# Optimization experiments

Hardware: AMD Instinct MI355X
Metric: run time of the kernel (lower is better)

## Reference

```python
import jax, jax.numpy as jnp
import numpy as np

H0, H1, NL, B, S = 2048, 1024, 8, 2, 2048

def _linear(x, w, b):
    return jnp.einsum('bsd,od->bso', x, w) + b

def setup_inputs() -> dict:
    key = jax.random.key(0)
    ks = jax.random.split(key, 32)
    d = {
        'z':    jax.random.normal(ks[0], (B, S, H0), jnp.float32),
        'act0': jax.random.normal(ks[1], (B, S, H0), jnp.float32),
        'act1': jax.random.normal(ks[2], (B, S, H0), jnp.float32),
        'attmask': jax.random.randint(ks[3], (B, S), 0, 2, jnp.int32),
        'dproj_w': jax.random.normal(ks[4], (H1, H0), jnp.float32) * 0.02,
        'dproj_b': jnp.zeros((H1,), jnp.float32),
        'uproj_w': jax.random.normal(ks[5], (H0, H1), jnp.float32) * 0.02,
        'uproj_b': jnp.zeros((H0,), jnp.float32),
        'wq_w': jax.random.normal(ks[6], (NL, H1, H1), jnp.float32) * 0.02,
        'wq_b': jnp.zeros((NL, H1), jnp.float32),
        'wk_w': jax.random.normal(ks[7], (NL, H1, H1), jnp.float32) * 0.02,
        'wk_b': jnp.zeros((NL, H1), jnp.float32),
        'wv_w': jax.random.normal(ks[8], (NL, H1, H1), jnp.float32) * 0.02,
        'wv_b': jnp.zeros((NL, H1), jnp.float32),
        'mlp1_w': jax.random.normal(ks[9], (NL, 4 * H1, H1), jnp.float32) * 0.02,
        'mlp1_b': jnp.zeros((NL, 4 * H1), jnp.float32),
        'mlp2_w': jax.random.normal(ks[10], (NL, H1, 4 * H1), jnp.float32) * 0.02,
        'mlp2_b': jnp.zeros((NL, H1), jnp.float32),
    }
    return d

def _ladder_fwd(z, act0, act1, attmask, dproj_w, dproj_b, uproj_w, uproj_b,
                wq_w, wq_b, wk_w, wk_b, wv_w, wv_b,
                mlp1_w, mlp1_b, mlp2_w, mlp2_b):
    seq = z.shape[1]
    scale = 1.0 / jnp.sqrt(jnp.float32(H1))
    causal = jnp.tril(jnp.ones((seq, seq), bool))  # [S,S]
    pad = (attmask != 0)[:, None, :]               # [B,1,S] key padding mask
    neg = jnp.float32(-1e9)

    def ladsatt(i, x):
        Q = _linear(x, wq_w[i], wq_b[i])
        K = _linear(x, wk_w[i], wk_b[i])
        V = _linear(x, wv_w[i], wv_b[i])
        scores = jnp.einsum('bqd,bkd->bqk', Q, K) * scale
        scores = jnp.where(causal[None], scores, neg)
        scores = jnp.where(pad, scores, neg)
        w = jax.nn.softmax(scores, axis=-1)
        return jnp.einsum('bqk,bkd->bqd', w, V)

    def mlp(i, x):
        h = jax.nn.relu(_linear(x, mlp1_w[i], mlp1_b[i]))
        return _linear(h, mlp2_w[i], mlp2_b[i])

    rs = _linear(act0, dproj_w, dproj_b)
    rs = rs + ladsatt(0, rs)
    rs = rs + mlp(0, rs)
    rs = rs + _linear(act1, dproj_w, dproj_b)
    rs = rs + ladsatt(1, rs)
    rs = rs + mlp(1, rs)
    for i in range(2, NL):
        rs = rs + ladsatt(i, rs)
        rs = rs + mlp(i, rs)
    return _linear(rs, uproj_w, uproj_b) + z

def reference(z, act0, act1, attmask, dproj_w, dproj_b, uproj_w, uproj_b,
              wq_w, wq_b, wk_w, wk_b, wv_w, wv_b,
              mlp1_w, mlp1_b, mlp2_w, mlp2_b):
    return _ladder_fwd(z, act0, act1, attmask, dproj_w, dproj_b, uproj_w, uproj_b,
                       wq_w, wq_b, wk_w, wk_b, wv_w, wv_b,
                       mlp1_w, mlp1_b, mlp2_w, mlp2_b)
```

## Files before the change

### kernel.cpp

```cpp
#include <hip/hip_runtime.h>
#include <cstdint>


typedef unsigned short u16;
typedef __attribute__((ext_vector_type(8))) __bf16 bf16x8;
typedef __attribute__((ext_vector_type(4))) float f32x4;

#define DI __device__ __forceinline__

constexpr int BB = 2, SSQ = 2048, HH0 = 2048, HH1 = 1024, NLAY = 8, HH4 = 4096;
constexpr int MM = BB * SSQ;

DI float bf2f(u16 h) {
  union { uint32_t u; float f; } x; x.u = ((uint32_t)h) << 16; return x.f;
}
DI u16 f2bf(float f) {
  union { float f; uint32_t u; } x; x.f = f;
  uint32_t u = x.u;
  return (u16)((u + 0x7fffu + ((u >> 16) & 1u)) >> 16);
}

enum {
  FB_BIAS = 1, FB_RES = 2, FB_RELU = 4, FB_F32 = 8, FB_SPLIT = 16,
  FB_CSKIP = 32, FB_CKLOOP = 64
};

template <int F, int KSP>
__global__ __launch_bounds__(256) void gemm_split(
    const u16* __restrict__ Ah, const u16* __restrict__ Al, long sAz, int lda,
    const u16* __restrict__ Bh, const u16* __restrict__ Bl, long sBz, int ldb,
    const float* __restrict__ bias, const float* __restrict__ resF,
    float* Cf, u16* Ch, u16* Cl, long sCz, int ldc, int K, long pstride) {
  int gx = gridDim.x, gy = gridDim.y, gz = gridDim.z;
  long o = blockIdx.x + (long)gx * (blockIdx.y + (long)gy * blockIdx.z);
  long nwg = (long)gx * gy * gz;
  long cq = nwg >> 3, cr = nwg & 7;
  long xcd = o & 7, cidx = o >> 3;
  long sl = (xcd < cr ? xcd * (cq + 1) : cr * (cq + 1) + (xcd - cr) * cq) + cidx;
  int bx = (int)(sl % gx);
  long tt = sl / gx;
  int by = (int)(tt % gy);
  int bzf = (int)(tt / gy);
  int NB = gz / KSP;
  int bz = bzf % NB;
  int ks = bzf / NB;

  if ((F & FB_CSKIP) && bx > by) return;

  __shared__ __align__(16) u16 Sbuf[2][4][128 * 32];

  int tid = threadIdx.x;
  int lane = tid & 63;
  int wave = tid >> 6;
  int wr = (wave >> 1) << 6;
  int wc = (wave & 1) << 6;
  int lrow = lane & 15;
  int kg = lane >> 4;
  int kc8 = (kg ^ ((lrow >> 1) & 3)) << 3;

  const u16* Abh = Ah + (long)bz * sAz + ((long)(by << 7)) * lda;
  const u16* Abl = Al + (long)bz * sAz + ((long)(by << 7)) * lda;
  const u16* Bbh = Bh + (long)bz * sBz + ((long)(bx << 7)) * ldb;
  const u16* Bbl = Bl + (long)bz * sBz + ((long)(bx << 7)) * ldb;

  int nKtot = (F & FB_CKLOOP) ? ((by + 1) << 2) : (K >> 5);
  int kbeg = (KSP > 1) ? (ks * nKtot) / KSP : 0;
  int kend = (KSP > 1) ? ((ks + 1) * nKtot) / KSP : nKtot;

  f32x4 acc[4][4] = {};

  auto STAGE = [&](int buf, int kt) {
    int k0 = kt << 5;
#pragma unroll
    for (int it = 0; it < 2; ++it) {
      int sidx = (it << 8) + tid;
      int r = sidx >> 2;
      int jsw = (sidx & 3) ^ ((r >> 1) & 3);
      long goff = (long)r * lda + (k0 + (jsw << 3));
      long gofB = (long)r * ldb + (k0 + (jsw << 3));
      int loff = sidx << 3;
      __builtin_amdgcn_global_load_lds(
          (__attribute__((address_space(1))) void*)(Abh + goff),
          (__attribute__((address_space(3))) void*)(&Sbuf[buf][0][loff]), 16, 0, 0);
      __builtin_amdgcn_global_load_lds(
          (__attribute__((address_space(1))) void*)(Abl + goff),
          (__attribute__((address_space(3))) void*)(&Sbuf[buf][1][loff]), 16, 0, 0);
      __builtin_amdgcn_global_load_lds(
          (__attribute__((address_space(1))) void*)(Bbh + gofB),
          (__attribute__((address_space(3))) void*)(&Sbuf[buf][2][loff]), 16, 0, 0);
      __builtin_amdgcn_global_load_lds(
          (__attribute__((address_space(1))) void*)(Bbl + gofB),
          (__attribute__((address_space(3))) void*)(&Sbuf[buf][3][loff]), 16, 0, 0);
    }
  };

  auto COMPUTE = [&](int buf) {
    bf16x8 afh[4], bfh[4], bfl[4];
#pragma unroll
    for (int mi = 0; mi < 4; ++mi)
      afh[mi] = *(const bf16x8*)&Sbuf[buf][0][((wr + (mi << 4) + lrow) << 5) + kc8];
#pragma unroll
    for (int ni = 0; ni < 4; ++ni) {
      bfh[ni] = *(const bf16x8*)&Sbuf[buf][2][((wc + (ni << 4) + lrow) << 5) + kc8];
      bfl[ni] = *(const bf16x8*)&Sbuf[buf][3][((wc + (ni << 4) + lrow) << 5) + kc8];
    }
#pragma unroll
    for (int mi = 0; mi < 4; ++mi)
#pragma unroll
      for (int ni = 0; ni < 4; ++ni) {
        acc[mi][ni] = __builtin_amdgcn_mfma_f32_16x16x32_bf16(
            afh[mi], bfh[ni], acc[mi][ni], 0, 0, 0);
        acc[mi][ni] = __builtin_amdgcn_mfma_f32_16x16x32_bf16(
            afh[mi], bfl[ni], acc[mi][ni], 0, 0, 0);
      }
    bf16x8 afl[4];
#pragma unroll
    for (int mi = 0; mi < 4; ++mi)
      afl[mi] = *(const bf16x8*)&Sbuf[buf][1][((wr + (mi << 4) + lrow) << 5) + kc8];
#pragma unroll
    for (int mi = 0; mi < 4; ++mi)
#pragma unroll
      for (int ni = 0; ni < 4; ++ni)
        acc[mi][ni] = __builtin_amdgcn_mfma_f32_16x16x32_bf16(
            afl[mi], bfh[ni], acc[mi][ni], 0, 0, 0);
  };

  STAGE(0, kbeg);
  int cur = 0;
  for (int kt = kbeg; kt < kend; ++kt) {
    bool more = (kt + 1 < kend);
    if (more) STAGE(cur ^ 1, kt + 1);
    if (more) asm volatile("s_waitcnt vmcnt(8)" ::: "memory");
    else      asm volatile("s_waitcnt vmcnt(0)" ::: "memory");
    __builtin_amdgcn_s_barrier();
    asm volatile("" ::: "memory");
    COMPUTE(cur);
    asm volatile("" ::: "memory");
    __builtin_amdgcn_s_barrier();
    asm volatile("" ::: "memory");
    cur ^= 1;
  }

  int m0 = (by << 7) + wr + (kg << 2);
  int n0 = (bx << 7) + wc;
#pragma unroll
  for (int mi = 0; mi < 4; ++mi) {
#pragma unroll
    for (int ni = 0; ni < 4; ++ni) {
      int col = n0 + (ni << 4) + lrow;
      float bv = 0.f;
      if ((KSP == 1) && (F & FB_BIAS)) bv = bias[col];
      int rb = m0 + (mi << 4);
#pragma unroll
      for (int r = 0; r < 4; ++r) {
        float v = acc[mi][ni][r];
        long ci = (long)bz * sCz + (long)(rb + r) * ldc + col;
        if constexpr (KSP > 1) {
          Cf[(long)ks * pstride + ci] = v;
        } else {
          v += bv;
          if (F & FB_RELU) v = fmaxf(v, 0.f);
          if (F & FB_RES) v += resF[ci];
          if (F & FB_F32) Cf[ci] = v;
          if (F & FB_SPLIT) {
            u16 h = f2bf(v);
            Ch[ci] = h;
            Cl[ci] = f2bf(v - bf2f(h));
          }
        }
      }
    }
  }
}

template <int F, int KSP>
__global__ __launch_bounds__(512, 2) void gemm_big(
    const u16* __restrict__ Ah, const u16* __restrict__ Al, int lda,
    const u16* __restrict__ Bh, const u16* __restrict__ Bl, int ldb,
    const float* __restrict__ bias,
    float* Cf, u16* Ch, u16* Cl, int ldc, int K, long pstride) {
  int gx = gridDim.x, gy = gridDim.y, gz = gridDim.z;
  long o = blockIdx.x + (long)gx * (blockIdx.y + (long)gy * blockIdx.z);
  long nwg = (long)gx * gy * gz;
  long cq = nwg >> 3, cr = nwg & 7;
  long xcd = o & 7, cidx = o >> 3;
  long sl = (xcd < cr ? xcd * (cq + 1) : cr * (cq + 1) + (xcd - cr) * cq) + cidx;
  int bx = (int)(sl % gx);
  long tt = sl / gx;
  int by = (int)(tt % gy);
  int ks = (int)(tt / gy);

  __shared__ __align__(16) u16 Sbuf[2][4][256 * 32];

  int tid = threadIdx.x;
  int lane = tid & 63;
  int wave = tid >> 6;
  int wm = (wave >> 2) << 7;
  int wn = (wave & 3) << 6;
  int lrow = lane & 15;
  int kg = lane >> 4;
  int kc8 = (kg ^ ((lrow >> 1) & 3)) << 3;

  const u16* Abh = Ah + ((long)(by << 8)) * lda;
  const u16* Abl = Al + ((long)(by << 8)) * lda;
  const u16* Bbh = Bh + ((long)(bx << 8)) * ldb;
  const u16* Bbl = Bl + ((long)(bx << 8)) * ldb;

  int nKtot = K >> 5;
  int kbeg = (KSP > 1) ? (ks * nKtot) / KSP : 0;
  int kend = (KSP > 1) ? ((ks + 1) * nKtot) / KSP : nKtot;

  f32x4 acc[8][4] = {};

  auto STAGE = [&](int buf, int kt) {
    int k0 = kt << 5;
#pragma unroll
    for (int it = 0; it < 2; ++it) {
      int sidx = (it << 9) + tid;
      int r = sidx >> 2;
      int jsw = (sidx & 3) ^ ((r >> 1) & 3);
      long goff = (long)r * lda + (k0 + (jsw << 3));
      long gofB = (long)r * ldb + (k0 + (jsw << 3));
      int loff = sidx << 3;
      __builtin_amdgcn_global_load_lds(
          (__attribute__((address_space(1))) void*)(Abh + goff),
          (__attribute__((address_space(3))) void*)(&Sbuf[buf][0][loff]), 16, 0, 0);
      __builtin_amdgcn_global_load_lds(
          (__attribute__((address_space(1))) void*)(Abl + goff),
          (__attribute__((address_space(3))) void*)(&Sbuf[buf][1][loff]), 16, 0, 0);
      __builtin_amdgcn_global_load_lds(
          (__attribute__((address_space(1))) void*)(Bbh + gofB),
          (__attribute__((address_space(3))) void*)(&Sbuf[buf][2][loff]), 16, 0, 0);
      __builtin_amdgcn_global_load_lds(
          (__attribute__((address_space(1))) void*)(Bbl + gofB),
          (__attribute__((address_space(3))) void*)(&Sbuf[buf][3][loff]), 16, 0, 0);
    }
  };

  auto COMPUTE = [&](int buf) {
    bf16x8 bfh[4], bfl[4];
#pragma unroll
    for (int ni = 0; ni < 4; ++ni) {
      int brow = wn + (ni << 4) + lrow;
      bfh[ni] = *(const bf16x8*)&Sbuf[buf][2][(brow << 5) + kc8];
      bfl[ni] = *(const bf16x8*)&Sbuf[buf][3][(brow << 5) + kc8];
    }
#pragma unroll
    for (int mi = 0; mi < 8; ++mi) {
      int arow = wm + (mi << 4) + lrow;
      bf16x8 ah = *(const bf16x8*)&Sbuf[buf][0][(arow << 5) + kc8];
      bf16x8 al = *(const bf16x8*)&Sbuf[buf][1][(arow << 5) + kc8];
#pragma unroll
      for (int ni = 0; ni < 4; ++ni) {
        acc[mi][ni] = __builtin_amdgcn_mfma_f32_16x16x32_bf16(
            ah, bfh[ni], acc[mi][ni], 0, 0, 0);
        acc[mi][ni] = __builtin_amdgcn_mfma_f32_16x16x32_bf16(
            ah, bfl[ni], acc[mi][ni], 0, 0, 0);
        acc[mi][ni] = __builtin_amdgcn_mfma_f32_16x16x32_bf16(
            al, bfh[ni], acc[mi][ni], 0, 0, 0);
      }
    }
  };

  STAGE(0, kbeg);
  int cur = 0;
  for (int kt = kbeg; kt < kend; ++kt) {
    bool more = (kt + 1 < kend);
    if (more) STAGE(cur ^ 1, kt + 1);
    if (more) asm volatile("s_waitcnt vmcnt(8)" ::: "memory");
    else      asm volatile("s_waitcnt vmcnt(0)" ::: "memory");
    __builtin_amdgcn_s_barrier();
    asm volatile("" ::: "memory");
    COMPUTE(cur);
    asm volatile("" ::: "memory");
    __builtin_amdgcn_s_barrier();
    asm volatile("" ::: "memory");
    cur ^= 1;
  }

  int m0 = (by << 8) + wm + (kg << 2);
  int n0 = (bx << 8) + wn;
#pragma unroll
  for (int mi = 0; mi < 8; ++mi) {
#pragma unroll
    for (int ni = 0; ni < 4; ++ni) {
      int col = n0 + (ni << 4) + lrow;
      float bv = 0.f;
      if ((KSP == 1) && (F & FB_BIAS)) bv = bias[col];
      int rb = m0 + (mi << 4);
#pragma unroll
      for (int r = 0; r < 4; ++r) {
        float v = acc[mi][ni][r];
        long ci = (long)(rb + r) * ldc + col;
        if constexpr (KSP > 1) {
          Cf[(long)ks * pstride + ci] = v;
        } else {
          v += bv;
          if (F & FB_RELU) v = fmaxf(v, 0.f);
          if (F & FB_F32) Cf[ci] = v;
          if (F & FB_SPLIT) {
            u16 h = f2bf(v);
            Ch[ci] = h;
            Cl[ci] = f2bf(v - bf2f(h));
          }
        }
      }
    }
  }
}

template <int KSP, bool RES>
__global__ void reduce_split(const float* __restrict__ p,
                             const float* __restrict__ bias,
                             float* __restrict__ rs, u16* __restrict__ xh,
                             u16* __restrict__ xl) {
  long i = ((long)blockIdx.x * 256 + threadIdx.x) << 2;
  int col = (int)(i & 1023);
  constexpr long PSTR = (long)MM * HH1;
  float4 v;
  v.x = bias[col]; v.y = bias[col + 1]; v.z = bias[col + 2]; v.w = bias[col + 3];
#pragma unroll
  for (int j = 0; j < KSP; ++j) {
    float4 a = *(const float4*)(p + i + j * PSTR);
    v.x += a.x; v.y += a.y; v.z += a.z; v.w += a.w;
  }
  if (RES) {
    float4 r0 = *(const float4*)(rs + i);
    v.x += r0.x; v.y += r0.y; v.z += r0.z; v.w += r0.w;
  }
  *(float4*)(rs + i) = v;
  ushort4 h, l;
  h.x = f2bf(v.x); l.x = f2bf(v.x - bf2f(h.x));
  h.y = f2bf(v.y); l.y = f2bf(v.y - bf2f(h.y));
  h.z = f2bf(v.z); l.z = f2bf(v.z - bf2f(h.z));
  h.w = f2bf(v.w); l.w = f2bf(v.w - bf2f(h.w));
  *(ushort4*)(xh + i) = h;
  *(ushort4*)(xl + i) = l;
}

__global__ void split_kernel(const float* __restrict__ src, u16* __restrict__ hi,
                             u16* __restrict__ lo) {
  long i = ((long)blockIdx.x * 256 + threadIdx.x) << 2;
  float4 v = *(const float4*)(src + i);
  ushort4 h, l;
  h.x = f2bf(v.x); l.x = f2bf(v.x - bf2f(h.x));
  h.y = f2bf(v.y); l.y = f2bf(v.y - bf2f(h.y));
  h.z = f2bf(v.z); l.z = f2bf(v.z - bf2f(h.z));
  h.w = f2bf(v.w); l.w = f2bf(v.w - bf2f(h.w));
  *(ushort4*)(hi + i) = h;
  *(ushort4*)(lo + i) = l;
}

__global__ void concat_bias(const float* __restrict__ qb, const float* __restrict__ kb,
                            const float* __restrict__ vb, float* __restrict__ dst) {
  int j = blockIdx.x * 256 + threadIdx.x;
  float v = (j < 1024) ? qb[j] : ((j < 2048) ? kb[j - 1024] : vb[j - 2048]);
  dst[j] = v;
}

__global__ void deg_kernel(const int* __restrict__ am, int* __restrict__ deg) {
  int i = blockIdx.x * 256 + threadIdx.x;
  int b = i >> 11, q = i & 2047;
  const int* a = am + b * SSQ;
  int any = 0;
  for (int k = 0; k <= q; ++k) any |= (a[k] != 0);
  deg[i] = !any;
}

__global__ void transpose_v2(const u16* __restrict__ Vh, const u16* __restrict__ Vl,
                             int sld, u16* __restrict__ VTh, u16* __restrict__ VTl) {
  __shared__ u16 th[64][68];
  __shared__ u16 tl[64][68];
  int b = blockIdx.z;
  int c0 = blockIdx.x << 6;
  int r0 = blockIdx.y << 6;
  int tr = threadIdx.x >> 4, tc = threadIdx.x & 15;
  long sbase = ((long)(b * SSQ + r0)) * sld + c0;
#pragma unroll
  for (int j = 0; j < 4; ++j) {
    int r = (j << 4) + tr;
    ushort4 uh = *(const ushort4*)(Vh + sbase + (long)r * sld + (tc << 2));
    ushort4 ul = *(const ushort4*)(Vl + sbase + (long)r * sld + (tc << 2));
    th[r][(tc << 2) + 0] = uh.x; th[r][(tc << 2) + 1] = uh.y;
    th[r][(tc << 2) + 2] = uh.z; th[r][(tc << 2) + 3] = uh.w;
    tl[r][(tc << 2) + 0] = ul.x; tl[r][(tc << 2) + 1] = ul.y;
    tl[r][(tc << 2) + 2] = ul.z; tl[r][(tc << 2) + 3] = ul.w;
  }
  __syncthreads();
  long dbase = ((long)b * HH1 + c0) * SSQ + r0;
#pragma unroll
  for (int j = 0; j < 4; ++j) {
    int c = (j << 4) + tr;
    ushort4 uh, ul;
    uh.x = th[(tc << 2) + 0][c]; uh.y = th[(tc << 2) + 1][c];
    uh.z = th[(tc << 2) + 2][c]; uh.w = th[(tc << 2) + 3][c];
    ul.x = tl[(tc << 2) + 0][c]; ul.y = tl[(tc << 2) + 1][c];
    ul.z = tl[(tc << 2) + 2][c]; ul.w = tl[(tc << 2) + 3][c];
    *(ushort4*)(VTh + dbase + (long)c * SSQ + (tc << 2)) = uh;
    *(ushort4*)(VTl + dbase + (long)c * SSQ + (tc << 2)) = ul;
  }
}

__global__ void colmean_partial(const u16* __restrict__ Vh, const u16* __restrict__ Vl,
                                int ld, float* __restrict__ part) {
  int n = blockIdx.x * 256 + threadIdx.x;
  int b = blockIdx.y, kc = blockIdx.z;
  long base = ((long)(b * SSQ + kc * 256)) * ld + n;
  float s = 0.f;
  for (int k = 0; k < 256; ++k) {
    long o = base + (long)k * ld;
    s += bf2f(Vh[o]) + bf2f(Vl[o]);
  }
  part[((kc * BB) + b) * HH1 + n] = s;
}
__global__ void colmean_final(const float* __restrict__ part, float* __restrict__ mV) {
  int i = blockIdx.x * 256 + threadIdx.x;
  int b = i >> 10, n = i & 1023;
  float s = 0.f;
  for (int kc = 0; kc < 8; ++kc) s += part[((kc * BB) + b) * HH1 + n];
  mV[i] = s * (1.f / (float)SSQ);
}

__global__ void softmax_kernel(const float* __restrict__ sc, u16* __restrict__ Ph,
                               u16* __restrict__ Pl, const int* __restrict__ am,
                               const int* __restrict__ deg) {
  int q = blockIdx.x, b = blockIdx.y;
  int tid = threadIdx.x;
  long rowoff = ((long)b * SSQ + q) * SSQ;
  int qt_end = ((q >> 7) + 1) << 7;
  if (deg[b * SSQ + q]) {
    for (int k = tid; k < qt_end; k += 256) { Ph[rowoff + k] = 0; Pl[rowoff + k] = 0; }
    return;
  }
  const int* a = am + b * SSQ;
  const float scale = 0.03125f;
  constexpr long PSTR = (long)BB * SSQ * SSQ;
  __shared__ float rowbuf[2048];
  __shared__ float sred[8];
  int w = tid >> 6, ln = tid & 63;

  for (int k = tid; k < qt_end; k += 256)
    rowbuf[k] = sc[rowoff + k] + sc[rowoff + k + PSTR];
  __syncthreads();

  float m = -1e30f;
  for (int k = tid; k <= q; k += 256)
    if (a[k]) m = fmaxf(m, rowbuf[k]);
#pragma unroll
  for (int o = 32; o; o >>= 1) m = fmaxf(m, __shfl_xor(m, o));
  if (!ln) sred[w] = m;
  __syncthreads();
  float M = fmaxf(fmaxf(sred[0], sred[1]), fmaxf(sred[2], sred[3]));

  float s = 0.f;
  for (int k = tid; k <= q; k += 256)
    if (a[k]) s += expf((rowbuf[k] - M) * scale);
#pragma unroll
  for (int o = 32; o; o >>= 1) s += __shfl_xor(s, o);
  if (!ln) sred[4 + w] = s;
  __syncthreads();
  float Ssum = sred[4] + sred[5] + sred[6] + sred[7];
  float inv = 1.f / Ssum;

  for (int k = tid; k < qt_end; k += 256) {
    float p = 0.f;
    if (k <= q && a[k]) p = expf((rowbuf[k] - M) * scale) * inv;
    u16 h = f2bf(p);
    Ph[rowoff + k] = h;
    Pl[rowoff + k] = f2bf(p - bf2f(h));
  }
}

__global__ void attn_post(float* __restrict__ rs, const float* __restrict__ pv,
                          u16* __restrict__ xh, u16* __restrict__ xl,
                          const int* __restrict__ deg, const float* __restrict__ mV) {
  long t = (long)blockIdx.x * 256 + threadIdx.x;
  long i = t << 2;
  int row = (int)(i >> 10);
  int col = (int)(i & 1023);
  int b = row >> 11;
  constexpr long PSTR = (long)BB * SSQ * HH1;
  float4 v = *(const float4*)(rs + i);
  float4 a = *(const float4*)(pv + i);
  float4 c = *(const float4*)(pv + i + PSTR);
  v.x += a.x + c.x; v.y += a.y + c.y; v.z += a.z + c.z; v.w += a.w + c.w;
  if (deg[row]) {
    const float* m = mV + (b << 10) + col;
    v.x += m[0]; v.y += m[1]; v.z += m[2]; v.w += m[3];
  }
  *(float4*)(rs + i) = v;
  ushort4 h, l;
  h.x = f2bf(v.x); l.x = f2bf(v.x - bf2f(h.x));
  h.y = f2bf(v.y); l.y = f2bf(v.y - bf2f(h.y));
  h.z = f2bf(v.z); l.z = f2bf(v.z - bf2f(h.z));
  h.w = f2bf(v.w); l.w = f2bf(v.w - bf2f(h.w));
  *(ushort4*)(xh + i) = h;
  *(ushort4*)(xl + i) = l;
}

constexpr size_t MB = 1u << 20;
constexpr size_t OFF_RS    = 0;
constexpr size_t OFF_XH    = 16 * MB;
constexpr size_t OFF_XL    = 24 * MB;
constexpr size_t OFF_QKVH  = 32 * MB;
constexpr size_t OFF_QKVL  = 56 * MB;
constexpr size_t OFF_PH    = 32 * MB;
constexpr size_t OFF_PL    = 48 * MB;
constexpr size_t OFF_RED   = 32 * MB;
constexpr size_t OFF_VTH   = 80 * MB;
constexpr size_t OFF_VTL   = 88 * MB;
constexpr size_t OFF_SC    = 96 * MB;
constexpr size_t OFF_ACTH  = 96 * MB;
constexpr size_t OFF_ACTL  = 112 * MB;
constexpr size_t OFF_HH    = 96 * MB;
constexpr size_t OFF_HL    = 128 * MB;
constexpr size_t OFF_PVP   = 128 * MB;
constexpr size_t OFF_DPWH  = 160 * MB;
constexpr size_t OFF_DPWL  = 164 * MB;
constexpr size_t OFF_UPWH  = 168 * MB;
constexpr size_t OFF_UPWL  = 172 * MB;
constexpr size_t OFF_WQKVH = 176 * MB;
constexpr size_t OFF_WQKVL = 182 * MB;
constexpr size_t OFF_M1H   = 188 * MB;
constexpr size_t OFF_M1L   = 196 * MB;
constexpr size_t OFF_M2H   = 204 * MB;
constexpr size_t OFF_M2L   = 212 * MB;
constexpr size_t OFF_QKVB  = 220 * MB;
constexpr size_t OFF_MV    = OFF_QKVB + 16 * 1024;
constexpr size_t OFF_PART  = OFF_MV + 16 * 1024;
constexpr size_t OFF_DEG   = OFF_PART + 128 * 1024;

extern "C" void kernel_launch(void* const* d_in, const int* in_sizes, int n_in,
                              void* d_out, int out_size, void* d_ws, size_t ws_size,
                              hipStream_t stream) {
  (void)in_sizes; (void)n_in; (void)out_size; (void)ws_size;

  const float* z    = (const float*)d_in[0];
  const float* act0 = (const float*)d_in[1];
  const float* act1 = (const float*)d_in[2];
  const int* amask  = (const int*)d_in[3];
  const float* dpw  = (const float*)d_in[4];
  const float* dpb  = (const float*)d_in[5];
  const float* upw  = (const float*)d_in[6];
  const float* upb  = (const float*)d_in[7];
  const float* wqw  = (const float*)d_in[8];
  const float* wqb  = (const float*)d_in[9];
  const float* wkw  = (const float*)d_in[10];
  const float* wkb  = (const float*)d_in[11];
  const float* wvw  = (const float*)d_in[12];
  const float* wvb  = (const float*)d_in[13];
  const float* m1w  = (const float*)d_in[14];
  const float* m1b  = (const float*)d_in[15];
  const float* m2w  = (const float*)d_in[16];
  const float* m2b  = (const float*)d_in[17];

  char* ws = (char*)d_ws;
  float* rs    = (float*)(ws + OFF_RS);
  u16* xh      = (u16*)(ws + OFF_XH);    u16* xl    = (u16*)(ws + OFF_XL);
  u16* qkvh    = (u16*)(ws + OFF_QKVH);  u16* qkvl  = (u16*)(ws + OFF_QKVL);
  u16* Ph      = (u16*)(ws + OFF_PH);    u16* Pl    = (u16*)(ws + OFF_PL);
  float* redp  = (float*)(ws + OFF_RED);
  u16* VTh     = (u16*)(ws + OFF_VTH);   u16* VTl   = (u16*)(ws + OFF_VTL);
  float* scb   = (float*)(ws + OFF_SC);
  u16* acth    = (u16*)(ws + OFF_ACTH);  u16* actl  = (u16*)(ws + OFF_ACTL);
  u16* hh      = (u16*)(ws + OFF_HH);    u16* hl    = (u16*)(ws + OFF_HL);
  float* pvp   = (float*)(ws + OFF_PVP);
  u16* dpwh    = (u16*)(ws + OFF_DPWH);  u16* dpwl  = (u16*)(ws + OFF_DPWL);
  u16* upwh    = (u16*)(ws + OFF_UPWH);  u16* upwl  = (u16*)(ws + OFF_UPWL);
  u16* wqkvh   = (u16*)(ws + OFF_WQKVH); u16* wqkvl = (u16*)(ws + OFF_WQKVL);
  u16* m1h     = (u16*)(ws + OFF_M1H);   u16* m1l   = (u16*)(ws + OFF_M1L);
  u16* m2h     = (u16*)(ws + OFF_M2H);   u16* m2l   = (u16*)(ws + OFF_M2L);
  float* qkvb  = (float*)(ws + OFF_QKVB);
  float* mV    = (float*)(ws + OFF_MV);
  float* part  = (float*)(ws + OFF_PART);
  int* deg     = (int*)(ws + OFF_DEG);

  constexpr long RPSTR = (long)MM * HH1;

  deg_kernel<<<dim3((BB * SSQ) / 256), 256, 0, stream>>>(amask, deg);
  split_kernel<<<dim3((HH1 * HH0) / 1024), 256, 0, stream>>>(dpw, dpwh, dpwl);
  split_kernel<<<dim3((HH0 * HH1) / 1024), 256, 0, stream>>>(upw, upwh, upwl);

  split_kernel<<<dim3((MM * HH0) / 1024), 256, 0, stream>>>(act0, acth, actl);
  gemm_big<0, 4><<<dim3(HH1 / 256, MM / 256, 4), 512, 0, stream>>>(
      acth, actl, HH0, dpwh, dpwl, HH0, nullptr,
      redp, nullptr, nullptr, HH1, HH0, RPSTR);
  reduce_split<4, false><<<dim3(MM * HH1 / 1024), 256, 0, stream>>>(
      redp, dpb, rs, xh, xl);

  for (int i = 0; i < NLAY; ++i) {
    split_kernel<<<dim3((HH1 * HH1) / 1024), 256, 0, stream>>>(
        wqw + (size_t)i * HH1 * HH1, wqkvh, wqkvl);
    split_kernel<<<dim3((HH1 * HH1) / 1024), 256, 0, stream>>>(
        wkw + (size_t)i * HH1 * HH1, wqkvh + HH1 * HH1, wqkvl + HH1 * HH1);
    split_kernel<<<dim3((HH1 * HH1) / 1024), 256, 0, stream>>>(
        wvw + (size_t)i * HH1 * HH1, wqkvh + 2 * HH1 * HH1, wqkvl + 2 * HH1 * HH1);
    concat_bias<<<dim3(12), 256, 0, stream>>>(wqb + i * HH1, wkb + i * HH1,
                                              wvb + i * HH1, qkvb);
    split_kernel<<<dim3((HH4 * HH1) / 1024), 256, 0, stream>>>(
        m1w + (size_t)i * HH4 * HH1, m1h, m1l);
    split_kernel<<<dim3((HH1 * HH4) / 1024), 256, 0, stream>>>(
        m2w + (size_t)i * HH1 * HH4, m2h, m2l);

    if (i == 1) {
      split_kernel<<<dim3((MM * HH0) / 1024), 256, 0, stream>>>(act1, acth, actl);
      gemm_big<0, 4><<<dim3(HH1 / 256, MM / 256, 4), 512, 0, stream>>>(
          acth, actl, HH0, dpwh, dpwl, HH0, nullptr,
          redp, nullptr, nullptr, HH1, HH0, RPSTR);
      reduce_split<4, true><<<dim3(MM * HH1 / 1024), 256, 0, stream>>>(
          redp, dpb, rs, xh, xl);
    }

    gemm_split<FB_BIAS | FB_SPLIT, 1><<<dim3(3072 / 128, MM / 128, 1), 256, 0, stream>>>(
        xh, xl, 0, HH1, wqkvh, wqkvl, 0, HH1, qkvb, nullptr,
        nullptr, qkvh, qkvl, 0, 3072, HH1, 0);

    transpose_v2<<<dim3(HH1 / 64, SSQ / 64, BB), 256, 0, stream>>>(
        qkvh + 2048, qkvl + 2048, 3072, VTh, VTl);
    colmean_partial<<<dim3(HH1 / 256, BB, 8), 256, 0, stream>>>(
        qkvh + 2048, qkvl + 2048, 3072, part);
    colmean_final<<<dim3((BB * HH1) / 256), 256, 0, stream>>>(part, mV);

    gemm_split<FB_CSKIP, 2><<<dim3(SSQ / 128, SSQ / 128, BB * 2), 256, 0, stream>>>(
        qkvh, qkvl, (long)SSQ * 3072, 3072, qkvh + 1024, qkvl + 1024,
        (long)SSQ * 3072, 3072, nullptr, nullptr,
        scb, nullptr, nullptr, (long)SSQ * SSQ, SSQ, HH1, (long)BB * SSQ * SSQ);

    softmax_kernel<<<dim3(SSQ, BB), 256, 0, stream>>>(scb, Ph, Pl, amask, deg);

    gemm_split<FB_CKLOOP, 2><<<dim3(HH1 / 128, SSQ / 128, BB * 2), 256, 0, stream>>>(
        Ph, Pl, (long)SSQ * SSQ, SSQ, VTh, VTl, (long)HH1 * SSQ, SSQ, nullptr, nullptr,
        pvp, nullptr, nullptr, (long)SSQ * HH1, HH1, SSQ, (long)BB * SSQ * HH1);

    attn_post<<<dim3((MM * HH1 / 4) / 256), 256, 0, stream>>>(rs, pvp, xh, xl, deg, mV);

    gemm_big<FB_BIAS | FB_RELU | FB_SPLIT, 1>
        <<<dim3(HH4 / 256, MM / 256, 1), 512, 0, stream>>>(
        xh, xl, HH1, m1h, m1l, HH1, m1b + i * HH4,
        nullptr, hh, hl, HH4, HH1, 0);
    gemm_big<0, 4><<<dim3(HH1 / 256, MM / 256, 4), 512, 0, stream>>>(
        hh, hl, HH4, m2h, m2l, HH4, nullptr,
        redp, nullptr, nullptr, HH1, HH4, RPSTR);
    reduce_split<4, true><<<dim3(MM * HH1 / 1024), 256, 0, stream>>>(
        redp, m2b + i * HH1, rs, xh, xl);
  }

  gemm_split<FB_BIAS | FB_RES | FB_F32, 1>
      <<<dim3(HH0 / 128, MM / 128, 1), 256, 0, stream>>>(
      xh, xl, 0, HH1, upwh, upwl, 0, HH1, upb, z,
      (float*)d_out, nullptr, nullptr, 0, HH0, HH1, 0);
}
```

Baseline: 3.922 ms.

## Interleave GEMM loads with MFMA phases, add setprio, optimize softmax and deg kernels

The big GEMM's main loop is split into four MFMA phases. Global-to-LDS loads for the next K tile are staggered between those phases, and each MFMA block is wrapped in s_setprio, so memory traffic overlaps compute instead of being issued all at once. The split GEMM also gets setprio around its MFMA blocks. The softmax caches exp values in shared memory so exp is not computed twice, and deg_kernel becomes a per-batch first-nonzero reduction instead of a quadratic per-query scan. The extra barriers per K step add synchronization cost and could offset the overlap gain.

```diff
diff --git a/kernel.cpp b/kernel.cpp
--- a/kernel.cpp
+++ b/kernel.cpp
@@ -24,6 +24,8 @@
   FB_BIAS = 1, FB_RES = 2, FB_RELU = 4, FB_F32 = 8, FB_SPLIT = 16,
   FB_CSKIP = 32, FB_CKLOOP = 64
 };
+
+#define MFMA_BF16 __builtin_amdgcn_mfma_f32_16x16x32_bf16
 
 template <int F, int KSP>
 __global__ __launch_bounds__(256) void gemm_split(
@@ -104,25 +106,26 @@
       bfh[ni] = *(const bf16x8*)&Sbuf[buf][2][((wc + (ni << 4) + lrow) << 5) + kc8];
       bfl[ni] = *(const bf16x8*)&Sbuf[buf][3][((wc + (ni << 4) + lrow) << 5) + kc8];
     }
+    __builtin_amdgcn_s_setprio(1);
 #pragma unroll
     for (int mi = 0; mi < 4; ++mi)
 #pragma unroll
       for (int ni = 0; ni < 4; ++ni) {
-        acc[mi][ni] = __builtin_amdgcn_mfma_f32_16x16x32_bf16(
-            afh[mi], bfh[ni], acc[mi][ni], 0, 0, 0);
-        acc[mi][ni] = __builtin_amdgcn_mfma_f32_16x16x32_bf16(
-            afh[mi], bfl[ni], acc[mi][ni], 0, 0, 0);
+        acc[mi][ni] = MFMA_BF16(afh[mi], bfh[ni], acc[mi][ni], 0, 0, 0);
+        acc[mi][ni] = MFMA_BF16(afh[mi], bfl[ni], acc[mi][ni], 0, 0, 0);
       }
+    __builtin_amdgcn_s_setprio(0);
     bf16x8 afl[4];
 #pragma unroll
     for (int mi = 0; mi < 4; ++mi)
       afl[mi] = *(const bf16x8*)&Sbuf[buf][1][((wr + (mi << 4) + lrow) << 5) + kc8];
+    __builtin_amdgcn_s_setprio(1);
 #pragma unroll
     for (int mi = 0; mi < 4; ++mi)
 #pragma unroll
       for (int ni = 0; ni < 4; ++ni)
-        acc[mi][ni] = __builtin_amdgcn_mfma_f32_16x16x32_bf16(
-            afl[mi], bfh[ni], acc[mi][ni], 0, 0, 0);
+        acc[mi][ni] = MFMA_BF16(afl[mi], bfh[ni], acc[mi][ni], 0, 0, 0);
+    __builtin_amdgcn_s_setprio(0);
   };
 
   STAGE(0, kbeg);
@@ -212,71 +215,80 @@
 
   f32x4 acc[8][4] = {};
 
-  auto STAGE = [&](int buf, int kt) {
-    int k0 = kt << 5;
-#pragma unroll
-    for (int it = 0; it < 2; ++it) {
-      int sidx = (it << 9) + tid;
-      int r = sidx >> 2;
-      int jsw = (sidx & 3) ^ ((r >> 1) & 3);
-      long goff = (long)r * lda + (k0 + (jsw << 3));
-      long gofB = (long)r * ldb + (k0 + (jsw << 3));
-      int loff = sidx << 3;
-      __builtin_amdgcn_global_load_lds(
-          (__attribute__((address_space(1))) void*)(Abh + goff),
-          (__attribute__((address_space(3))) void*)(&Sbuf[buf][0][loff]), 16, 0, 0);
-      __builtin_amdgcn_global_load_lds(
-          (__attribute__((address_space(1))) void*)(Abl + goff),
-          (__attribute__((address_space(3))) void*)(&Sbuf[buf][1][loff]), 16, 0, 0);
-      __builtin_amdgcn_global_load_lds(
-          (__attribute__((address_space(1))) void*)(Bbh + gofB),
-          (__attribute__((address_space(3))) void*)(&Sbuf[buf][2][loff]), 16, 0, 0);
-      __builtin_amdgcn_global_load_lds(
-          (__attribute__((address_space(1))) void*)(Bbl + gofB),
-          (__attribute__((address_space(3))) void*)(&Sbuf[buf][3][loff]), 16, 0, 0);
-    }
-  };
-
-  auto COMPUTE = [&](int buf) {
-    bf16x8 bfh[4], bfl[4];
-#pragma unroll
-    for (int ni = 0; ni < 4; ++ni) {
-      int brow = wn + (ni << 4) + lrow;
-      bfh[ni] = *(const bf16x8*)&Sbuf[buf][2][(brow << 5) + kc8];
-      bfl[ni] = *(const bf16x8*)&Sbuf[buf][3][(brow << 5) + kc8];
-    }
-#pragma unroll
-    for (int mi = 0; mi < 8; ++mi) {
-      int arow = wm + (mi << 4) + lrow;
-      bf16x8 ah = *(const bf16x8*)&Sbuf[buf][0][(arow << 5) + kc8];
-      bf16x8 al = *(const bf16x8*)&Sbuf[buf][1][(arow << 5) + kc8];
-#pragma unroll
-      for (int ni = 0; ni < 4; ++ni) {
-        acc[mi][ni] = __builtin_amdgcn_mfma_f32_16x16x32_bf16(
-            ah, bfh[ni], acc[mi][ni], 0, 0, 0);
-        acc[mi][ni] = __builtin_amdgcn_mfma_f32_16x16x32_bf16(
-            ah, bfl[ni], acc[mi][ni], 0, 0, 0);
-        acc[mi][ni] = __builtin_amdgcn_mfma_f32_16x16x32_bf16(
-            al, bfh[ni], acc[mi][ni], 0, 0, 0);
-      }
-    }
-  };
-
-  STAGE(0, kbeg);
+#define LOAD1(BUF, KT, IT, ST, BASE, LD) do {                                  \
+    int sidx_ = ((IT) << 9) + tid;                                             \
+    int r_ = sidx_ >> 2;                                                       \
+    int jsw_ = (sidx_ & 3) ^ ((r_ >> 1) & 3);                                  \
+    long off_ = (long)r_ * (LD) + (((KT) << 5) + (jsw_ << 3));                 \
+    __builtin_amdgcn_global_load_lds(                                          \
+        (__attribute__((address_space(1))) void*)((BASE) + off_),              \
+        (__attribute__((address_space(3))) void*)(&Sbuf[BUF][ST][sidx_ << 3]), \
+        16, 0, 0);                                                             \
+  } while (0)
+
+#define PHASE_MFMA(BUF, MI0) do {                                              \
+    int a0r_ = ((wm + ((MI0) << 4) + lrow) << 5) + kc8;                        \
+    int a1r_ = ((wm + (((MI0) + 1) << 4) + lrow) << 5) + kc8;                  \
+    bf16x8 a0h_ = *(const bf16x8*)&Sbuf[BUF][0][a0r_];                         \
+    bf16x8 a0l_ = *(const bf16x8*)&Sbuf[BUF][1][a0r_];                         \
+    bf16x8 a1h_ = *(const bf16x8*)&Sbuf[BUF][0][a1r_];                         \
+    bf16x8 a1l_ = *(const bf16x8*)&Sbuf[BUF][1][a1r_];                         \
+    __builtin_amdgcn_s_setprio(1);                                             \
+    _Pragma("unroll")                                                          \
+    for (int ni = 0; ni < 4; ++ni) {                                           \
+      acc[MI0][ni]     = MFMA_BF16(a0h_, bfh[ni], acc[MI0][ni], 0, 0, 0);      \
+      acc[MI0][ni]     = MFMA_BF16(a0h_, bfl[ni], acc[MI0][ni], 0, 0, 0);      \
+      acc[MI0][ni]     = MFMA_BF16(a0l_, bfh[ni], acc[MI0][ni], 0, 0, 0);      \
+      acc[MI0 + 1][ni] = MFMA_BF16(a1h_, bfh[ni], acc[MI0 + 1][ni], 0, 0, 0);  \
+      acc[MI0 + 1][ni] = MFMA_BF16(a1h_, bfl[ni], acc[MI0 + 1][ni], 0, 0, 0);  \
+      acc[MI0 + 1][ni] = MFMA_BF16(a1l_, bfh[ni], acc[MI0 + 1][ni], 0, 0, 0);  \
+    }                                                                          \
+    __builtin_amdgcn_s_setprio(0);                                             \
+  } while (0)
+
+#define BAR() do {                                                             \
+    asm volatile("" ::: "memory");                                             \
+    __builtin_amdgcn_s_barrier();                                              \
+    asm volatile("" ::: "memory");                                             \
+  } while (0)
+
+  {
+    LOAD1(0, kbeg, 0, 0, Abh, lda); LOAD1(0, kbeg, 0, 1, Abl, lda);
+    LOAD1(0, kbeg, 0, 2, Bbh, ldb); LOAD1(0, kbeg, 0, 3, Bbl, ldb);
+    LOAD1(0, kbeg, 1, 0, Abh, lda); LOAD1(0, kbeg, 1, 1, Abl, lda);
+    LOAD1(0, kbeg, 1, 2, Bbh, ldb); LOAD1(0, kbeg, 1, 3, Bbl, ldb);
+  }
   int cur = 0;
   for (int kt = kbeg; kt < kend; ++kt) {
     bool more = (kt + 1 < kend);
-    if (more) STAGE(cur ^ 1, kt + 1);
-    if (more) asm volatile("s_waitcnt vmcnt(8)" ::: "memory");
+    int nb = cur ^ 1, kt1 = kt + 1;
+    bf16x8 bfh[4], bfl[4];
+    if (more) { LOAD1(nb, kt1, 0, 0, Abh, lda); LOAD1(nb, kt1, 0, 1, Abl, lda); }
+    if (more) asm volatile("s_waitcnt vmcnt(2)" ::: "memory");
     else      asm volatile("s_waitcnt vmcnt(0)" ::: "memory");
-    __builtin_amdgcn_s_barrier();
-    asm volatile("" ::: "memory");
-    COMPUTE(cur);
-    asm volatile("" ::: "memory");
-    __builtin_amdgcn_s_barrier();
-    asm volatile("" ::: "memory");
+    BAR();
+#pragma unroll
+    for (int ni = 0; ni < 4; ++ni) {
+      int brow = (wn + (ni << 4) + lrow) << 5;
+      bfh[ni] = *(const bf16x8*)&Sbuf[cur][2][brow + kc8];
+      bfl[ni] = *(const bf16x8*)&Sbuf[cur][3][brow + kc8];
+    }
+    PHASE_MFMA(cur, 0);
+    BAR();
+    if (more) { LOAD1(nb, kt1, 0, 2, Bbh, ldb); LOAD1(nb, kt1, 0, 3, Bbl, ldb); }
+    PHASE_MFMA(cur, 2);
+    BAR();
+    if (more) { LOAD1(nb, kt1, 1, 0, Abh, lda); LOAD1(nb, kt1, 1, 1, Abl, lda); }
+    PHASE_MFMA(cur, 4);
+    BAR();
+    if (more) { LOAD1(nb, kt1, 1, 2, Bbh, ldb); LOAD1(nb, kt1, 1, 3, Bbl, ldb); }
+    PHASE_MFMA(cur, 6);
+    BAR();
     cur ^= 1;
   }
+#undef LOAD1
+#undef PHASE_MFMA
+#undef BAR
 
   int m0 = (by << 8) + wm + (kg << 2);
   int n0 = (bx << 8) + wn;
@@ -359,12 +371,19 @@
 }
 
 __global__ void deg_kernel(const int* __restrict__ am, int* __restrict__ deg) {
-  int i = blockIdx.x * 256 + threadIdx.x;
-  int b = i >> 11, q = i & 2047;
+  int b = blockIdx.x;
   const int* a = am + b * SSQ;
-  int any = 0;
-  for (int k = 0; k <= q; ++k) any |= (a[k] != 0);
-  deg[i] = !any;
+  int tid = threadIdx.x;
+  int fz = SSQ;
+  for (int k = tid; k < SSQ; k += 256)
+    if (a[k] != 0) fz = min(fz, k);
+#pragma unroll
+  for (int o = 32; o; o >>= 1) fz = min(fz, __shfl_xor(fz, o));
+  __shared__ int red[4];
+  if ((tid & 63) == 0) red[tid >> 6] = fz;
+  __syncthreads();
+  int f = min(min(red[0], red[1]), min(red[2], red[3]));
+  for (int q = tid; q < SSQ; q += 256) deg[b * SSQ + q] = (q < f) ? 1 : 0;
 }
 
 __global__ void transpose_v2(const u16* __restrict__ Vh, const u16* __restrict__ Vl,
@@ -453,8 +472,12 @@
   float M = fmaxf(fmaxf(sred[0], sred[1]), fmaxf(sred[2], sred[3]));
 
   float s = 0.f;
-  for (int k = tid; k <= q; k += 256)
-    if (a[k]) s += expf((rowbuf[k] - M) * scale);
+  for (int k = tid; k < qt_end; k += 256) {
+    float p = 0.f;
+    if (k <= q && a[k]) p = expf((rowbuf[k] - M) * scale);
+    rowbuf[k] = p;
+    s += p;
+  }
 #pragma unroll
   for (int o = 32; o; o >>= 1) s += __shfl_xor(s, o);
   if (!ln) sred[4 + w] = s;
@@ -463,8 +486,7 @@
   float inv = 1.f / Ssum;
 
   for (int k = tid; k < qt_end; k += 256) {
-    float p = 0.f;
-    if (k <= q && a[k]) p = expf((rowbuf[k] - M) * scale) * inv;
+    float p = rowbuf[k] * inv;
     u16 h = f2bf(p);
     Ph[rowoff + k] = h;
     Pl[rowoff + k] = f2bf(p - bf2f(h));
@@ -577,7 +599,7 @@
 
   constexpr long RPSTR = (long)MM * HH1;
 
-  deg_kernel<<<dim3((BB * SSQ) / 256), 256, 0, stream>>>(amask, deg);
+  deg_kernel<<<dim3(BB), 256, 0, stream>>>(amask, deg);
   split_kernel<<<dim3((HH1 * HH0) / 1024), 256, 0, stream>>>(dpw, dpwh, dpwl);
   split_kernel<<<dim3((HH0 * HH1) / 1024), 256, 0, stream>>>(upw, upwh, upwl);
 
```

New measurement: 3.753 ms. 4.3% less time.
